# Performance work log

Hardware: AMD Instinct MI355X
Metric: run time of the kernel (lower is better)

Reference implementation:

```python
import jax, jax.numpy as jnp
import numpy as np

B, L, D, H = 4, 1024, 256, 8
TEMP = float(np.sqrt(D))
EPS_SM = 1e-6
EPS_LN = 1e-5


def setup_inputs() -> dict:
    key = jax.random.key(0)
    ks = jax.random.split(key, 8)
    std = float(np.sqrt(2.0 / (D * 2)))
    return {
        "q": jax.random.normal(ks[0], (B, L, D), jnp.float32),
        "mask": jax.random.randint(ks[1], (B, L, L), 0, 2, jnp.int32),
        "k": jax.random.normal(ks[2], (B, L, D), jnp.float32),
        "v": jax.random.normal(ks[3], (B, L, D), jnp.float32),
        "w_qs": jax.random.normal(ks[4], (H * D, D), jnp.float32) * std,
        "w_ks": jax.random.normal(ks[5], (H * D, D), jnp.float32) * std,
        "w_vs": jax.random.normal(ks[6], (H * D, D), jnp.float32) * std,
        "fc_w": jax.random.normal(ks[7], (D, H * D), jnp.float32) * float(np.sqrt(2.0 / (D + H * D))),
        "fc_b": jnp.zeros((D,), jnp.float32),
        "ln_g": jnp.ones((D,), jnp.float32),
        "ln_b": jnp.zeros((D,), jnp.float32),
    }


def masked_softmax(x, m):
    # repo's layers.masked_softmax: clamp, mask-mul, stable exp, mask-mul, normalize
    x = jnp.clip(x, -15.0, 15.0) * m
    e = jnp.exp(x - jnp.max(x, axis=-1, keepdims=True)) * m
    return e / (jnp.sum(e, axis=-1, keepdims=True) + EPS_SM)


def reference(q, mask, k, v, w_qs, w_ks, w_vs, fc_w, fc_b, ln_g, ln_b):
    residual = q
    m = mask.astype(q.dtype)[:, None, :, :]          # [B,1,Lq,Lk]
    # projections to per-head full-dim: [B,L,H,D]
    qh = (q @ w_qs.T).reshape(B, L, H, D)
    kh = (k @ w_ks.T).reshape(B, L, H, D)
    vh = (v @ w_vs.T).reshape(B, L, H, D)
    scores = jnp.einsum("bqhd,bkhd->bhqk", qh, kh) / TEMP   # [B,H,Lq,Lk]
    attn = masked_softmax(scores, m)
    out = jnp.einsum("bhqk,bkhd->bqhd", attn, vh).reshape(B, L, H * D)
    out = out @ fc_w.T + fc_b                         # [B,L,D]
    out = out + residual
    mu = jnp.mean(out, axis=-1, keepdims=True)
    var = jnp.var(out, axis=-1, keepdims=True)
    out = (out - mu) / jnp.sqrt(var + EPS_LN) * ln_g + ln_b
    # match torch attn layout: [H*B, Lq, Lk] (head-major)
    attn_hb = jnp.transpose(attn, (1, 0, 2, 3)).reshape(H * B, L, L)
    return out, attn_hb
```

## Files before the change

### kernel.cpp

```cpp
#include <hip/hip_runtime.h>
#include <cstdint>
#include <math.h>

#define Bsz 4
#define Lsz 1024
#define Dsz 256
#define Hsz 8
#define HD  2048
#define NROWS (Bsz*Lsz)
#define INV_TEMP 0.0625f

typedef __attribute__((ext_vector_type(8))) short bf16x8;
typedef __attribute__((ext_vector_type(4))) float f32x4;

__device__ inline unsigned short f2bf(float f) {
    union { float f; unsigned u; } x; x.f = f;
    unsigned r = x.u + 0x7fffu + ((x.u >> 16) & 1u);
    return (unsigned short)(r >> 16);
}
__device__ inline float bf2f(unsigned short u) {
    union { unsigned u; float f; } x; x.u = (unsigned)u << 16; return x.f;
}

#define GBL(p) ((const __attribute__((address_space(1))) unsigned int*)(p))
#define LDS(p) ((__attribute__((address_space(3))) unsigned int*)(p))

template<int N> __device__ __forceinline__ void vmw() {
    if constexpr (N == 0)       asm volatile("s_waitcnt vmcnt(0)"  ::: "memory");
    else if constexpr (N == 3)  asm volatile("s_waitcnt vmcnt(3)"  ::: "memory");
    else if constexpr (N == 6)  asm volatile("s_waitcnt vmcnt(6)"  ::: "memory");
    else if constexpr (N == 10) asm volatile("s_waitcnt vmcnt(10)" ::: "memory");
    else if constexpr (N == 19) asm volatile("s_waitcnt vmcnt(19)" ::: "memory");
    else static_assert(N == 0, "unsupported vmcnt literal");
}

template <int TMv, int TNv, typename OutT, int EPI, int MINW, bool FUSE,
          int GX, int GY, int GZ>
__global__ __launch_bounds__(256, MINW) void gemm_bt(
    const unsigned short* __restrict__ A, const unsigned short* __restrict__ Bm,
    OutT* __restrict__ C,
    int K, int lda, int ldb, int ldc, int inner,
    long long sA1, long long sA2, long long sB1, long long sB2,
    long long sC1, long long sC2, float alpha,
    const unsigned short* __restrict__ A2, const unsigned short* __restrict__ B2,
    unsigned short* __restrict__ C2)
{
    constexpr int WMv = TMv / 2, WNv = TNv / 2;
    constexpr int IT = TMv / 32, JT = TNv / 32;
    constexpr int APASS = TMv / 32, NPASS = (TMv + TNv) / 32;
    constexpr int TILE = (TMv + TNv) * 64;
    constexpr int G = GX * GY * GZ;
    static_assert(G % 8 == 0, "bijective XCD swizzle needs G%8==0");
    static_assert(NPASS == 6, "vmcnt literal assumes NPASS==6");
    static_assert(TMv * (TNv + 4) * 4 <= 2 * TILE * 2, "epilogue LDS overflow");

    const int lid = blockIdx.x + GX * (blockIdx.y + GY * blockIdx.z);
    const int nid = (lid & 7) * (G >> 3) + (lid >> 3);
    int mx = nid % GX;
    const int t1g = nid / GX;
    int my = t1g % GY;
    const int zz = t1g / GY;

    if constexpr (FUSE) {
        if (zz >= 2) {
            const int idx = my * 64 + mx;
            if (idx >= 256) return;
            mx = idx & 31; my = idx >> 5;
            const int b = zz - 2;
            A   = A2;
            Bm  = B2 + (size_t)b * ((size_t)Lsz * Dsz);
            C   = (OutT*)(C2 + (size_t)b * ((size_t)HD * Lsz));
            ldc = Lsz;
        } else {
            A  += (size_t)zz * sA2;
            Bm += (size_t)zz * sB2;
            C  += (size_t)zz * sC2;
        }
    } else {
        const int i1 = zz / inner;
        const int i2 = zz % inner;
        A  += (size_t)i1 * sA1 + (size_t)i2 * sA2;
        Bm += (size_t)i1 * sB1 + (size_t)i2 * sB2;
        C  += (size_t)i1 * sC1 + (size_t)i2 * sC2;
    }

    __shared__ unsigned short S[2 * TILE];

    const int t    = threadIdx.x;
    const int lane = t & 63;
    const int w    = t >> 6;
    const int wm   = w & 1;
    const int wn   = w >> 1;
    const int m0   = mx * TMv;
    const int n0   = my * TNv;

    const int rA = t >> 3;
    const int ch = ((t & 7) ^ (rA & 7)) * 8;
    const unsigned short* gA = A  + (size_t)(m0 + rA) * lda + ch;
    const unsigned short* gB = Bm + (size_t)(n0 + rA) * ldb + ch;

    const int fr = lane & 15;
    const int q  = lane >> 4;

    f32x4 acc[IT][JT];
#pragma unroll
    for (int i = 0; i < IT; ++i)
#pragma unroll
        for (int j = 0; j < JT; ++j) acc[i][j] = (f32x4){0.f, 0.f, 0.f, 0.f};

    auto stage = [&](unsigned short* Sb, int k0) {
#pragma unroll
        for (int p = 0; p < NPASS; ++p) {
            const unsigned short* src = (p < APASS)
                ? (gA + (size_t)p * 32 * lda + k0)
                : (gB + (size_t)(p - APASS) * 32 * ldb + k0);
            __builtin_amdgcn_global_load_lds(GBL(src), LDS(Sb + p * 2048 + t * 8), 16, 0, 0);
        }
    };
    auto kstep = [&](const unsigned short* As) {
        const unsigned short* Bs = As + TMv * 64;
#pragma unroll
        for (int ks = 0; ks < 2; ++ks) {
            const int slot = ((ks * 4 + q) ^ (fr & 7)) * 8;
            bf16x8 a[IT], b[JT];
#pragma unroll
            for (int i = 0; i < IT; ++i)
                a[i] = *(const bf16x8*)(As + (wm * WMv + i * 16 + fr) * 64 + slot);
#pragma unroll
            for (int j = 0; j < JT; ++j)
                b[j] = *(const bf16x8*)(Bs + (wn * WNv + j * 16 + fr) * 64 + slot);
#pragma unroll
            for (int i = 0; i < IT; ++i)
#pragma unroll
                for (int j = 0; j < JT; ++j)
                    acc[i][j] = __builtin_amdgcn_mfma_f32_16x16x32_bf16(a[i], b[j], acc[i][j], 0, 0, 0);
        }
    };

    const int nk = K >> 6;
    stage(S, 0);

    for (int kt = 0; kt < nk; ++kt) {
        if (kt + 1 < nk) stage(S + ((kt + 1) & 1) * TILE, (kt + 1) << 6);
        if (kt + 1 < nk) vmw<6>(); else vmw<0>();
        __builtin_amdgcn_s_barrier();
        kstep(S + (kt & 1) * TILE);
        asm volatile("s_waitcnt lgkmcnt(0)" ::: "memory");
        __builtin_amdgcn_s_barrier();
    }

    {
        float* Lf = (float*)S;
        constexpr int LP = TNv + 4;
#pragma unroll
        for (int i = 0; i < IT; ++i)
#pragma unroll
            for (int j = 0; j < JT; ++j) {
                const int col = wn * WNv + j * 16 + fr;
#pragma unroll
                for (int r = 0; r < 4; ++r) {
                    const int row = wm * WMv + i * 16 + q * 4 + r;
                    Lf[row * LP + col] = acc[i][j][r] * alpha;
                }
            }
        __syncthreads();

        constexpr int SEGS = TNv / 32;
        constexpr int RPI  = 256 / SEGS;
#pragma unroll
        for (int it2 = 0; it2 < TMv / RPI; ++it2) {
            const int row = it2 * RPI + t / SEGS;
            const int c0  = (t % SEGS) * 32;
            const float* src = Lf + row * LP + c0;
            if constexpr (sizeof(OutT) == 4) {
                float* dst = (float*)C + (size_t)(m0 + row) * ldc + n0 + c0;
#pragma unroll
                for (int v4 = 0; v4 < 8; ++v4)
                    *(f32x4*)(dst + v4 * 4) = *(const f32x4*)(src + v4 * 4);
            } else {
                unsigned short* dst = (unsigned short*)C + (size_t)(m0 + row) * ldc + n0 + c0;
#pragma unroll
                for (int v8 = 0; v8 < 4; ++v8) {
                    bf16x8 o;
#pragma unroll
                    for (int e = 0; e < 8; ++e) o[e] = (short)f2bf(src[v8 * 8 + e]);
                    *(bf16x8*)(dst + v8 * 8) = o;
                }
            }
        }
    }
}

__global__ __launch_bounds__(256, 1) void attn_fused(
    const unsigned short* __restrict__ qh,
    const unsigned short* __restrict__ kh,
    const unsigned short* __restrict__ vt,
    const unsigned char*  __restrict__ maskb,
    unsigned short* __restrict__ e,
    unsigned short* __restrict__ attnv,
    float* __restrict__ attn)
{
    constexpr int G = 16 * 32;
    const int lid = blockIdx.x + 16 * blockIdx.z;
    const int nid = (lid & 7) * (G >> 3) + (lid >> 3);
    const int mx = nid & 15;
    const int z  = nid >> 4;
    const int h = z >> 2, b = z & 3;
    const int m0 = mx * 64;

    const unsigned short* gQ = qh + (size_t)b * Lsz * HD + (size_t)h * Dsz;
    const unsigned short* gK = kh + (size_t)b * Lsz * HD + (size_t)h * Dsz;
    const unsigned short* gV = vt + (size_t)b * HD * Lsz + (size_t)h * Dsz * Lsz;
    const unsigned char*  gM = maskb + (size_t)b * Lsz * Lsz;
    unsigned short* gE = e + (size_t)h * Bsz * Lsz * Lsz + (size_t)b * Lsz * Lsz;
    float* gA = attn + (size_t)z * Lsz * Lsz;

    __shared__ unsigned short S[69632];
    __shared__ float rs[64];
    unsigned short* KH = S;
    unsigned short* VT = S + 32768;
    unsigned short* P  = S + 65536;

    const int t = threadIdx.x;
    const int lane = t & 63;
    const int w = t >> 6;
    const int wm = w & 1, wn = w >> 1;
    const int fr = lane & 15, q = lane >> 4;

    if (t < 64) rs[t] = 0.f;

    bf16x8 Qr[2][8];
#pragma unroll
    for (int i = 0; i < 2; ++i) {
        const unsigned short* qrow = gQ + (size_t)(m0 + wm * 32 + i * 16 + fr) * HD;
#pragma unroll
        for (int ks = 0; ks < 8; ++ks)
            Qr[i][ks] = *(const bf16x8*)(qrow + ks * 32 + q * 8);
    }

    auto stageKH = [&](unsigned short* dst, int k0) {
#pragma unroll
        for (int p = 0; p < 8; ++p) {
            const int row = p * 8 + (t >> 5);
            const int c = t & 31;
            const int cs = (c & 24) | ((c & 7) ^ (row & 7));
            const unsigned short* src = gK + (size_t)(k0 + row) * HD + cs * 8;
            __builtin_amdgcn_global_load_lds(GBL(src), LDS(dst + p * 2048 + t * 8), 16, 0, 0);
        }
    };
    auto stageVT = [&](unsigned short* dst, int k0) {
#pragma unroll
        for (int p = 0; p < 8; ++p) {
            const int row = p * 32 + (t >> 3);
            const int cs = (t & 7) ^ (row & 7);
            const unsigned short* src = gV + (size_t)row * Lsz + k0 + cs * 8;
            __builtin_amdgcn_global_load_lds(GBL(src), LDS(dst + p * 2048 + t * 8), 16, 0, 0);
        }
    };

    f32x4 O[2][8];
#pragma unroll
    for (int i = 0; i < 2; ++i)
#pragma unroll
        for (int j = 0; j < 8; ++j) O[i][j] = (f32x4){0.f, 0.f, 0.f, 0.f};

    stageKH(KH, 0); stageVT(VT, 0);
    vmw<0>();
    __syncthreads();

    const int rowB = t >> 2, segB = t & 3;

    for (int kt = 0; kt < 16; ++kt) {
        const int cur = kt & 1;
        const unsigned char* mp = gM + (size_t)(m0 + rowB) * Lsz + kt * 64 + segB * 16;
        union { uint4 v; unsigned char c[16]; } mu;
        mu.v = *(const uint4*)mp;
        if (kt + 1 < 16) {
            stageKH(KH + (cur ^ 1) * 16384, (kt + 1) * 64);
            stageVT(VT + (cur ^ 1) * 16384, (kt + 1) * 64);
        }
        if (kt + 1 < 16) vmw<19>(); else vmw<3>();
        __builtin_amdgcn_s_barrier();

        const unsigned short* KHc = KH + cur * 16384;
        f32x4 Sa[2][2];
#pragma unroll
        for (int i = 0; i < 2; ++i)
#pragma unroll
            for (int j = 0; j < 2; ++j) Sa[i][j] = (f32x4){0.f, 0.f, 0.f, 0.f};
#pragma unroll
        for (int ks = 0; ks < 8; ++ks) {
            const int c = ks * 4 + q;
            const int cs = (c & 24) | ((c & 7) ^ (fr & 7));
            bf16x8 bfr[2];
#pragma unroll
            for (int j = 0; j < 2; ++j)
                bfr[j] = *(const bf16x8*)(KHc + (wn * 32 + j * 16 + fr) * 256 + cs * 8);
#pragma unroll
            for (int i = 0; i < 2; ++i)
#pragma unroll
                for (int j = 0; j < 2; ++j)
                    Sa[i][j] = __builtin_amdgcn_mfma_f32_16x16x32_bf16(Qr[i][ks], bfr[j], Sa[i][j], 0, 0, 0);
        }

#pragma unroll
        for (int i = 0; i < 2; ++i)
#pragma unroll
            for (int r = 0; r < 4; ++r) {
                const int row = wm * 32 + i * 16 + q * 4 + r;
#pragma unroll
                for (int j = 0; j < 2; ++j) {
                    const int col = wn * 32 + j * 16 + fr;
                    float vv = Sa[i][j][r] * INV_TEMP;
                    vv = __expf(fminf(fmaxf(vv, -15.f), 15.f));
                    P[row * 64 + (((col >> 3) ^ (row & 7)) * 8) + (col & 7)] = f2bf(vv);
                }
            }
        asm volatile("s_waitcnt lgkmcnt(0)" ::: "memory");
        __builtin_amdgcn_s_barrier();

        {
            const int c2a = (segB * 2) ^ (rowB & 7);
            const int c2b = (segB * 2 + 1) ^ (rowB & 7);
            bf16x8 p0 = *(const bf16x8*)(P + rowB * 64 + c2a * 8);
            bf16x8 p1 = *(const bf16x8*)(P + rowB * 64 + c2b * 8);
            float part = 0.f;
#pragma unroll
            for (int e2 = 0; e2 < 8; ++e2) {
                if (!mu.c[e2])     p0[e2] = 0;
                if (!mu.c[8 + e2]) p1[e2] = 0;
                part += bf2f((unsigned short)p0[e2]) + bf2f((unsigned short)p1[e2]);
            }
            unsigned short* ep = gE + (size_t)(m0 + rowB) * Lsz + kt * 64 + segB * 16;
            *(bf16x8*)ep = p0;
            *(bf16x8*)(ep + 8) = p1;
            *(bf16x8*)(P + rowB * 64 + c2a * 8) = p0;
            *(bf16x8*)(P + rowB * 64 + c2b * 8) = p1;
            part += __shfl_xor(part, 1, 64);
            part += __shfl_xor(part, 2, 64);
            if (segB == 0) rs[rowB] += part;
        }
        asm volatile("s_waitcnt lgkmcnt(0)" ::: "memory");
        __builtin_amdgcn_s_barrier();

        const unsigned short* VTc = VT + cur * 16384;
#pragma unroll
        for (int ks2 = 0; ks2 < 2; ++ks2) {
            const int cs = ((ks2 * 4 + q) ^ (fr & 7)) * 8;
            bf16x8 a2[2];
#pragma unroll
            for (int i = 0; i < 2; ++i)
                a2[i] = *(const bf16x8*)(P + (wm * 32 + i * 16 + fr) * 64 + cs);
#pragma unroll
            for (int j = 0; j < 8; ++j) {
                bf16x8 b2 = *(const bf16x8*)(VTc + (wn * 128 + j * 16 + fr) * 64 + cs);
#pragma unroll
                for (int i = 0; i < 2; ++i)
                    O[i][j] = __builtin_amdgcn_mfma_f32_16x16x32_bf16(a2[i], b2, O[i][j], 0, 0, 0);
            }
        }
        asm volatile("s_waitcnt lgkmcnt(0)" ::: "memory");
        __builtin_amdgcn_s_barrier();
    }

    if (t < 64) rs[t] = 1.0f / (rs[t] + 1e-6f);
    __syncthreads();

    {
        float* Lf = (float*)S;
#pragma unroll
        for (int i = 0; i < 2; ++i)
#pragma unroll
            for (int j = 0; j < 8; ++j) {
                const int col = wn * 128 + j * 16 + fr;
#pragma unroll
                for (int r = 0; r < 4; ++r)
                    Lf[(wm * 32 + i * 16 + q * 4 + r) * 260 + col] = O[i][j][r];
            }
        __syncthreads();
#pragma unroll
        for (int it2 = 0; it2 < 2; ++it2) {
            const int row = it2 * 32 + (t >> 3);
            const int c0 = (t & 7) * 32;
            const float iv = rs[row];
            const float* src = Lf + row * 260 + c0;
            unsigned short* dst = attnv + ((size_t)b * Lsz + m0 + row) * HD + h * Dsz + c0;
#pragma unroll
            for (int v8 = 0; v8 < 4; ++v8) {
                bf16x8 o;
#pragma unroll
                for (int e2 = 0; e2 < 8; ++e2) o[e2] = (short)f2bf(src[v8 * 8 + e2] * iv);
                *(bf16x8*)(dst + v8 * 8) = o;
            }
        }
    }

    vmw<0>();
    {
        const float iv = rs[rowB];
        const unsigned short* ebase = gE + (size_t)(m0 + rowB) * Lsz + segB * 16;
        float* abase = gA + (size_t)(m0 + rowB) * Lsz + segB * 16;
#pragma unroll 4
        for (int kt = 0; kt < 16; ++kt) {
            const unsigned short* ep = ebase + kt * 64;
            uint4 u0 = *(const uint4*)ep;
            uint4 u1 = *(const uint4*)(ep + 8);
            f32x4 f0, f1, f2, f3;
            f0.x = bf2f((unsigned short)(u0.x & 0xffff)) * iv; f0.y = bf2f((unsigned short)(u0.x >> 16)) * iv;
            f0.z = bf2f((unsigned short)(u0.y & 0xffff)) * iv; f0.w = bf2f((unsigned short)(u0.y >> 16)) * iv;
            f1.x = bf2f((unsigned short)(u0.z & 0xffff)) * iv; f1.y = bf2f((unsigned short)(u0.z >> 16)) * iv;
            f1.z = bf2f((unsigned short)(u0.w & 0xffff)) * iv; f1.w = bf2f((unsigned short)(u0.w >> 16)) * iv;
            f2.x = bf2f((unsigned short)(u1.x & 0xffff)) * iv; f2.y = bf2f((unsigned short)(u1.x >> 16)) * iv;
            f2.z = bf2f((unsigned short)(u1.y & 0xffff)) * iv; f2.w = bf2f((unsigned short)(u1.y >> 16)) * iv;
            f3.x = bf2f((unsigned short)(u1.z & 0xffff)) * iv; f3.y = bf2f((unsigned short)(u1.z >> 16)) * iv;
            f3.z = bf2f((unsigned short)(u1.w & 0xffff)) * iv; f3.w = bf2f((unsigned short)(u1.w >> 16)) * iv;
            float* ap = abase + kt * 64;
            *(f32x4*)ap = f0; *(f32x4*)(ap + 4) = f1;
            *(f32x4*)(ap + 8) = f2; *(f32x4*)(ap + 12) = f3;
        }
    }
}

__global__ __launch_bounds__(256) void cast_all(
    const float* __restrict__ q, const float* __restrict__ k, const float* __restrict__ v,
    const float* __restrict__ wq, const float* __restrict__ wk, const float* __restrict__ wv,
    const float* __restrict__ fw, const int* __restrict__ mask,
    unsigned short* __restrict__ qb, unsigned short* __restrict__ kb, unsigned short* __restrict__ vb,
    unsigned short* __restrict__ wqb, unsigned short* __restrict__ wkb, unsigned short* __restrict__ wvb,
    unsigned short* __restrict__ fwb, unsigned char* __restrict__ mb)
{
    const int gid = blockIdx.x * 256 + threadIdx.x;
    const int NQ = 262144;
    const int NW = 131072;
    const int NF = 3 * NQ + 4 * NW;
    if (gid >= NF) {
        const int off = gid - NF;
        const int4 mi = ((const int4*)mask)[off];
        uchar4 o;
        o.x = mi.x ? 1 : 0;
        o.y = mi.y ? 1 : 0;
        o.z = mi.z ? 1 : 0;
        o.w = mi.w ? 1 : 0;
        ((uchar4*)mb)[off] = o;
        return;
    }
    const float* src; unsigned short* dst; int off;
    if      (gid < NQ)            { src = q;  dst = qb;  off = gid; }
    else if (gid < 2 * NQ)        { src = k;  dst = kb;  off = gid - NQ; }
    else if (gid < 3 * NQ)        { src = v;  dst = vb;  off = gid - 2 * NQ; }
    else if (gid < 3 * NQ + NW)   { src = wq; dst = wqb; off = gid - 3 * NQ; }
    else if (gid < 3 * NQ + 2*NW) { src = wk; dst = wkb; off = gid - 3 * NQ - NW; }
    else if (gid < 3 * NQ + 3*NW) { src = wv; dst = wvb; off = gid - 3 * NQ - 2 * NW; }
    else                          { src = fw; dst = fwb; off = gid - 3 * NQ - 3 * NW; }
    float4 f = ((const float4*)src)[off];
    ushort4 o;
    o.x = f2bf(f.x); o.y = f2bf(f.y); o.z = f2bf(f.z); o.w = f2bf(f.w);
    ((ushort4*)dst)[off] = o;
}

__global__ __launch_bounds__(256) void ln_kernel(const float* __restrict__ gout,
                                                 const float* __restrict__ qin,
                                                 const float* __restrict__ fc_b,
                                                 const float* __restrict__ ln_g,
                                                 const float* __restrict__ ln_b,
                                                 float* __restrict__ out)
{
    const int row = blockIdx.x;
    const int t = threadIdx.x;
    const size_t idx = (size_t)row * Dsz + t;
    const size_t P = (size_t)NROWS * Dsz;
    const float val = gout[idx] + gout[idx + P] + gout[idx + 2 * P] + gout[idx + 3 * P]
                    + fc_b[t] + qin[idx];

    __shared__ float red[4];
    float s = val;
#pragma unroll
    for (int o = 32; o > 0; o >>= 1) s += __shfl_down(s, o, 64);
    const int lane = t & 63, w = t >> 6;
    if (lane == 0) red[w] = s;
    __syncthreads();
    const float mu = (red[0] + red[1] + red[2] + red[3]) * (1.0f / Dsz);
    __syncthreads();

    float d = val - mu;
    float s2 = d * d;
#pragma unroll
    for (int o = 32; o > 0; o >>= 1) s2 += __shfl_down(s2, o, 64);
    if (lane == 0) red[w] = s2;
    __syncthreads();
    const float var = (red[0] + red[1] + red[2] + red[3]) * (1.0f / Dsz);

    out[idx] = d * rsqrtf(var + 1e-5f) * ln_g[t] + ln_b[t];
}

extern "C" void kernel_launch(void* const* d_in, const int* in_sizes, int n_in,
                              void* d_out, int out_size, void* d_ws, size_t ws_size,
                              hipStream_t stream)
{
    const float* q    = (const float*)d_in[0];
    const int*   mask = (const int*)d_in[1];
    const float* k    = (const float*)d_in[2];
    const float* v    = (const float*)d_in[3];
    const float* w_qs = (const float*)d_in[4];
    const float* w_ks = (const float*)d_in[5];
    const float* w_vs = (const float*)d_in[6];
    const float* fc_w = (const float*)d_in[7];
    const float* fc_b = (const float*)d_in[8];
    const float* ln_g = (const float*)d_in[9];
    const float* ln_b = (const float*)d_in[10];

    float* out  = (float*)d_out;
    float* attn = (float*)d_out + (size_t)NROWS * Dsz;

    unsigned short* wsu = (unsigned short*)d_ws;
    unsigned short* qh     = wsu;
    unsigned short* kh     = qh + (size_t)NROWS * HD;
    unsigned short* q_bf   = kh + (size_t)NROWS * HD;
    unsigned short* k_bf   = q_bf + (size_t)NROWS * Dsz;
    unsigned short* v_bf   = k_bf + (size_t)NROWS * Dsz;
    unsigned short* wq_bf  = v_bf + (size_t)NROWS * Dsz;
    unsigned short* wk_bf  = wq_bf + (size_t)HD * Dsz;
    unsigned short* wv_bf  = wk_bf + (size_t)HD * Dsz;
    unsigned short* vt     = wv_bf + (size_t)HD * Dsz;
    unsigned short* attn_e = vt + (size_t)Bsz * HD * Lsz;
    unsigned short* attnv  = attn_e + (size_t)32 * Lsz * Lsz;
    unsigned short* fcw_bf = attnv + (size_t)NROWS * HD;
    float*          fcout  = (float*)(fcw_bf + (size_t)Dsz * HD);
    unsigned char*  maskb  = (unsigned char*)(fcout + (size_t)4 * NROWS * Dsz);

    dim3 blk(256);

    cast_all<<<dim3(9216), blk, 0, stream>>>(q, k, v, w_qs, w_ks, w_vs, fc_w, mask,
                                             q_bf, k_bf, v_bf, wq_bf, wk_bf, wv_bf, fcw_bf, maskb);

    {
        dim3 grid(NROWS / 64, HD / 128, 6);
        gemm_bt<64, 128, unsigned short, 0, 3, true, 64, 16, 6><<<grid, blk, 0, stream>>>(
            q_bf, wq_bf, qh,
            Dsz, Dsz, Dsz, HD, 2,
            0, (long long)NROWS * Dsz, 0, (long long)HD * Dsz, 0, (long long)NROWS * HD,
            1.0f,
            wv_bf, v_bf, vt);
    }

    attn_fused<<<dim3(16, 1, 32), blk, 0, stream>>>(qh, kh, vt, maskb, attn_e, attnv, attn);

    {
        dim3 grid(NROWS / 64, Dsz / 128, 4);
        gemm_bt<64, 128, float, 0, 3, false, 64, 2, 4><<<grid, blk, 0, stream>>>(
            attnv, fcw_bf, fcout,
            512, HD, HD, Dsz, 4,
            0, 512, 0, 512, 0, (long long)NROWS * Dsz,
            1.0f,
            nullptr, nullptr, nullptr);
    }

    ln_kernel<<<dim3(NROWS), blk, 0, stream>>>(fcout, q, fc_b, ln_g, ln_b, out);
}
```

Before: 373.2 us.

## Restructure fused attention for two blocks per CU with smaller K tiles

Shrinks the fused attention kernel's key tile from 64 to 32 columns, halving LDS use so two blocks can reside per CU (launch bounds raised to 2). Each wave now owns 16 full query rows across all 256 output columns, which removes one barrier per iteration. The mask is staged into LDS through async global-to-LDS loads alongside K and V instead of per-thread global loads. The trade-off is twice as many loop iterations, each with less MFMA work per barrier, and more register pressure from 16 output accumulators under the tighter occupancy bound.

```diff
diff --git a/kernel.cpp b/kernel.cpp
--- a/kernel.cpp
+++ b/kernel.cpp
@@ -27,10 +27,10 @@
 
 template<int N> __device__ __forceinline__ void vmw() {
     if constexpr (N == 0)       asm volatile("s_waitcnt vmcnt(0)"  ::: "memory");
-    else if constexpr (N == 3)  asm volatile("s_waitcnt vmcnt(3)"  ::: "memory");
+    else if constexpr (N == 1)  asm volatile("s_waitcnt vmcnt(1)"  ::: "memory");
     else if constexpr (N == 6)  asm volatile("s_waitcnt vmcnt(6)"  ::: "memory");
     else if constexpr (N == 10) asm volatile("s_waitcnt vmcnt(10)" ::: "memory");
-    else if constexpr (N == 19) asm volatile("s_waitcnt vmcnt(19)" ::: "memory");
+    else if constexpr (N == 11) asm volatile("s_waitcnt vmcnt(11)" ::: "memory");
     else static_assert(N == 0, "unsupported vmcnt literal");
 }
 
@@ -191,7 +191,7 @@
     }
 }
 
-__global__ __launch_bounds__(256, 1) void attn_fused(
+__global__ __launch_bounds__(256, 2) void attn_fused(
     const unsigned short* __restrict__ qh,
     const unsigned short* __restrict__ kh,
     const unsigned short* __restrict__ vt,
@@ -212,155 +212,123 @@
     const unsigned short* gK = kh + (size_t)b * Lsz * HD + (size_t)h * Dsz;
     const unsigned short* gV = vt + (size_t)b * HD * Lsz + (size_t)h * Dsz * Lsz;
     const unsigned char*  gM = maskb + (size_t)b * Lsz * Lsz;
-    unsigned short* gE = e + (size_t)h * Bsz * Lsz * Lsz + (size_t)b * Lsz * Lsz;
+    unsigned short* gE = e + (size_t)z * Lsz * Lsz;
     float* gA = attn + (size_t)z * Lsz * Lsz;
 
-    __shared__ unsigned short S[69632];
+    __shared__ unsigned short S[36864];
     __shared__ float rs[64];
-    unsigned short* KH = S;
-    unsigned short* VT = S + 32768;
-    unsigned short* P  = S + 65536;
+    unsigned short* P = S + 32768;
 
     const int t = threadIdx.x;
     const int lane = t & 63;
     const int w = t >> 6;
-    const int wm = w & 1, wn = w >> 1;
     const int fr = lane & 15, q = lane >> 4;
 
     if (t < 64) rs[t] = 0.f;
 
-    bf16x8 Qr[2][8];
-#pragma unroll
-    for (int i = 0; i < 2; ++i) {
-        const unsigned short* qrow = gQ + (size_t)(m0 + wm * 32 + i * 16 + fr) * HD;
+    bf16x8 Qr[8];
+    {
+        const unsigned short* qrow = gQ + (size_t)(m0 + w * 16 + fr) * HD;
 #pragma unroll
         for (int ks = 0; ks < 8; ++ks)
-            Qr[i][ks] = *(const bf16x8*)(qrow + ks * 32 + q * 8);
-    }
-
-    auto stageKH = [&](unsigned short* dst, int k0) {
-#pragma unroll
-        for (int p = 0; p < 8; ++p) {
+            Qr[ks] = *(const bf16x8*)(qrow + ks * 32 + q * 8);
+    }
+
+    auto stageTile = [&](int buf, int kt) {
+        unsigned short* KHd = S + buf * 8192;
+        unsigned short* VTd = S + 16384 + buf * 8192;
+        unsigned char*  Md  = (unsigned char*)(S + 34816) + buf * 2048;
+        const int k0 = kt * 32;
+#pragma unroll
+        for (int p = 0; p < 4; ++p) {
             const int row = p * 8 + (t >> 5);
             const int c = t & 31;
             const int cs = (c & 24) | ((c & 7) ^ (row & 7));
-            const unsigned short* src = gK + (size_t)(k0 + row) * HD + cs * 8;
-            __builtin_amdgcn_global_load_lds(GBL(src), LDS(dst + p * 2048 + t * 8), 16, 0, 0);
+            __builtin_amdgcn_global_load_lds(GBL(gK + (size_t)(k0 + row) * HD + cs * 8),
+                                             LDS(KHd + p * 2048 + t * 8), 16, 0, 0);
+        }
+#pragma unroll
+        for (int p = 0; p < 4; ++p) {
+            const int row = p * 64 + (t >> 2);
+            const int cs = (t & 3) ^ ((t >> 3) & 3);
+            __builtin_amdgcn_global_load_lds(GBL(gV + (size_t)row * Lsz + k0 + cs * 8),
+                                             LDS(VTd + p * 2048 + t * 8), 16, 0, 0);
+        }
+#pragma unroll
+        for (int p = 0; p < 2; ++p) {
+            const int mrow = p * 32 + (t >> 3);
+            const int mcol = (t & 7) * 4;
+            __builtin_amdgcn_global_load_lds(GBL(gM + (size_t)(m0 + mrow) * Lsz + k0 + mcol),
+                                             LDS(Md + p * 1024 + t * 4), 4, 0, 0);
         }
     };
-    auto stageVT = [&](unsigned short* dst, int k0) {
-#pragma unroll
-        for (int p = 0; p < 8; ++p) {
-            const int row = p * 32 + (t >> 3);
-            const int cs = (t & 7) ^ (row & 7);
-            const unsigned short* src = gV + (size_t)row * Lsz + k0 + cs * 8;
-            __builtin_amdgcn_global_load_lds(GBL(src), LDS(dst + p * 2048 + t * 8), 16, 0, 0);
-        }
-    };
-
-    f32x4 O[2][8];
-#pragma unroll
-    for (int i = 0; i < 2; ++i)
-#pragma unroll
-        for (int j = 0; j < 8; ++j) O[i][j] = (f32x4){0.f, 0.f, 0.f, 0.f};
-
-    stageKH(KH, 0); stageVT(VT, 0);
-    vmw<0>();
-    __syncthreads();
-
-    const int rowB = t >> 2, segB = t & 3;
-
-    for (int kt = 0; kt < 16; ++kt) {
+
+    f32x4 O[16];
+#pragma unroll
+    for (int j = 0; j < 16; ++j) O[j] = (f32x4){0.f, 0.f, 0.f, 0.f};
+
+    stageTile(0, 0);
+
+    for (int kt = 0; kt < 32; ++kt) {
         const int cur = kt & 1;
-        const unsigned char* mp = gM + (size_t)(m0 + rowB) * Lsz + kt * 64 + segB * 16;
-        union { uint4 v; unsigned char c[16]; } mu;
-        mu.v = *(const uint4*)mp;
-        if (kt + 1 < 16) {
-            stageKH(KH + (cur ^ 1) * 16384, (kt + 1) * 64);
-            stageVT(VT + (cur ^ 1) * 16384, (kt + 1) * 64);
-        }
-        if (kt + 1 < 16) vmw<19>(); else vmw<3>();
+        if (kt + 1 < 32) stageTile(cur ^ 1, kt + 1);
+        if (kt + 1 < 32) { if (kt >= 1) vmw<11>(); else vmw<10>(); }
+        else vmw<1>();
         __builtin_amdgcn_s_barrier();
 
-        const unsigned short* KHc = KH + cur * 16384;
-        f32x4 Sa[2][2];
-#pragma unroll
-        for (int i = 0; i < 2; ++i)
-#pragma unroll
-            for (int j = 0; j < 2; ++j) Sa[i][j] = (f32x4){0.f, 0.f, 0.f, 0.f};
+        const unsigned short* KHc = S + cur * 8192;
+        const unsigned short* VTc = S + 16384 + cur * 8192;
+        const unsigned char*  Mc  = (const unsigned char*)(S + 34816) + cur * 2048;
+
+        f32x4 Sa[2] = {(f32x4){0.f,0.f,0.f,0.f}, (f32x4){0.f,0.f,0.f,0.f}};
 #pragma unroll
         for (int ks = 0; ks < 8; ++ks) {
             const int c = ks * 4 + q;
             const int cs = (c & 24) | ((c & 7) ^ (fr & 7));
-            bf16x8 bfr[2];
-#pragma unroll
-            for (int j = 0; j < 2; ++j)
-                bfr[j] = *(const bf16x8*)(KHc + (wn * 32 + j * 16 + fr) * 256 + cs * 8);
-#pragma unroll
-            for (int i = 0; i < 2; ++i)
-#pragma unroll
-                for (int j = 0; j < 2; ++j)
-                    Sa[i][j] = __builtin_amdgcn_mfma_f32_16x16x32_bf16(Qr[i][ks], bfr[j], Sa[i][j], 0, 0, 0);
-        }
-
-#pragma unroll
-        for (int i = 0; i < 2; ++i)
+#pragma unroll
+            for (int j = 0; j < 2; ++j) {
+                bf16x8 bfr = *(const bf16x8*)(KHc + (j * 16 + fr) * 256 + cs * 8);
+                Sa[j] = __builtin_amdgcn_mfma_f32_16x16x32_bf16(Qr[ks], bfr, Sa[j], 0, 0, 0);
+            }
+        }
+
+#pragma unroll
+        for (int j = 0; j < 2; ++j)
 #pragma unroll
             for (int r = 0; r < 4; ++r) {
-                const int row = wm * 32 + i * 16 + q * 4 + r;
-#pragma unroll
-                for (int j = 0; j < 2; ++j) {
-                    const int col = wn * 32 + j * 16 + fr;
-                    float vv = Sa[i][j][r] * INV_TEMP;
-                    vv = __expf(fminf(fmaxf(vv, -15.f), 15.f));
-                    P[row * 64 + (((col >> 3) ^ (row & 7)) * 8) + (col & 7)] = f2bf(vv);
-                }
+                const int row = w * 16 + q * 4 + r;
+                const int col = j * 16 + fr;
+                float vv = Sa[j][r] * INV_TEMP;
+                vv = __expf(fminf(fmaxf(vv, -15.f), 15.f));
+                P[row * 32 + (((j * 2 + (fr >> 3)) ^ q) * 8) + (fr & 7)]
+                    = Mc[row * 32 + col] ? f2bf(vv) : (unsigned short)0;
             }
         asm volatile("s_waitcnt lgkmcnt(0)" ::: "memory");
-        __builtin_amdgcn_s_barrier();
 
         {
-            const int c2a = (segB * 2) ^ (rowB & 7);
-            const int c2b = (segB * 2 + 1) ^ (rowB & 7);
-            bf16x8 p0 = *(const bf16x8*)(P + rowB * 64 + c2a * 8);
-            bf16x8 p1 = *(const bf16x8*)(P + rowB * 64 + c2b * 8);
+            const int rowB = w * 16 + (lane >> 2);
+            const int segB = lane & 3;
+            const int cch = segB ^ ((lane >> 4) & 3);
+            bf16x8 p0 = *(const bf16x8*)(P + rowB * 32 + cch * 8);
             float part = 0.f;
 #pragma unroll
-            for (int e2 = 0; e2 < 8; ++e2) {
-                if (!mu.c[e2])     p0[e2] = 0;
-                if (!mu.c[8 + e2]) p1[e2] = 0;
-                part += bf2f((unsigned short)p0[e2]) + bf2f((unsigned short)p1[e2]);
-            }
-            unsigned short* ep = gE + (size_t)(m0 + rowB) * Lsz + kt * 64 + segB * 16;
-            *(bf16x8*)ep = p0;
-            *(bf16x8*)(ep + 8) = p1;
-            *(bf16x8*)(P + rowB * 64 + c2a * 8) = p0;
-            *(bf16x8*)(P + rowB * 64 + c2b * 8) = p1;
+            for (int e2 = 0; e2 < 8; ++e2) part += bf2f((unsigned short)p0[e2]);
+            *(bf16x8*)(gE + (size_t)(m0 + rowB) * Lsz + kt * 32 + segB * 8) = p0;
             part += __shfl_xor(part, 1, 64);
             part += __shfl_xor(part, 2, 64);
             if (segB == 0) rs[rowB] += part;
         }
+
+        {
+            bf16x8 a2 = *(const bf16x8*)(P + (w * 16 + fr) * 32 + ((q ^ ((fr >> 2) & 3)) * 8));
+#pragma unroll
+            for (int j = 0; j < 16; ++j) {
+                bf16x8 b2 = *(const bf16x8*)(VTc + (j * 16 + fr) * 32 + ((q ^ ((fr >> 1) & 3)) * 8));
+                O[j] = __builtin_amdgcn_mfma_f32_16x16x32_bf16(a2, b2, O[j], 0, 0, 0);
+            }
+        }
         asm volatile("s_waitcnt lgkmcnt(0)" ::: "memory");
         __builtin_amdgcn_s_barrier();
-
-        const unsigned short* VTc = VT + cur * 16384;
-#pragma unroll
-        for (int ks2 = 0; ks2 < 2; ++ks2) {
-            const int cs = ((ks2 * 4 + q) ^ (fr & 7)) * 8;
-            bf16x8 a2[2];
-#pragma unroll
-            for (int i = 0; i < 2; ++i)
-                a2[i] = *(const bf16x8*)(P + (wm * 32 + i * 16 + fr) * 64 + cs);
-#pragma unroll
-            for (int j = 0; j < 8; ++j) {
-                bf16x8 b2 = *(const bf16x8*)(VTc + (wn * 128 + j * 16 + fr) * 64 + cs);
-#pragma unroll
-                for (int i = 0; i < 2; ++i)
-                    O[i][j] = __builtin_amdgcn_mfma_f32_16x16x32_bf16(a2[i], b2, O[i][j], 0, 0, 0);
-            }
-        }
-        asm volatile("s_waitcnt lgkmcnt(0)" ::: "memory");
-        __builtin_amdgcn_s_barrier();
     }
 
     if (t < 64) rs[t] = 1.0f / (rs[t] + 1e-6f);
@@ -369,14 +337,10 @@
     {
         float* Lf = (float*)S;
 #pragma unroll
-        for (int i = 0; i < 2; ++i)
-#pragma unroll
-            for (int j = 0; j < 8; ++j) {
-                const int col = wn * 128 + j * 16 + fr;
-#pragma unroll
-                for (int r = 0; r < 4; ++r)
-                    Lf[(wm * 32 + i * 16 + q * 4 + r) * 260 + col] = O[i][j][r];
-            }
+        for (int j = 0; j < 16; ++j)
+#pragma unroll
+            for (int r = 0; r < 4; ++r)
+                Lf[(w * 16 + q * 4 + r) * 260 + j * 16 + fr] = O[j][r];
         __syncthreads();
 #pragma unroll
         for (int it2 = 0; it2 < 2; ++it2) {
@@ -397,6 +361,8 @@
 
     vmw<0>();
     {
+        const int rowB = t >> 2;
+        const int segB = t & 3;
         const float iv = rs[rowB];
         const unsigned short* ebase = gE + (size_t)(m0 + rowB) * Lsz + segB * 16;
         float* abase = gA + (size_t)(m0 + rowB) * Lsz + segB * 16;
```

Measured after the change: 356.9 us. 4.4% less time.
